# Kernel optimization log

Hardware: AMD Instinct MI355X
Metric: run time of the kernel (lower is better)

Reference implementation:

```python
import jax, jax.numpy as jnp
import numpy as np

NUM_GRAPHS = 100  # batch of graphs for pooling (dgl.max_nodes / WeightAndSum)


def _glorot(k, shape):
    lim = np.sqrt(6.0 / (shape[0] + shape[1])).astype(np.float32)
    return jax.random.uniform(k, shape, jnp.float32, -lim, lim)


def setup_inputs() -> dict:
    key = jax.random.key(0)
    ks = jax.random.split(key, 10)
    N, E, D, H = 100000, 1600000, 128, 128
    node_feats = jax.random.normal(ks[0], (N, D), dtype=jnp.float32)
    src = jax.random.randint(ks[1], (E,), 0, N, dtype=jnp.int32)
    dst = jax.random.randint(ks[2], (E,), 0, N, dtype=jnp.int32)
    graph_ids = jnp.sort(jax.random.randint(ks[3], (N,), 0, NUM_GRAPHS, dtype=jnp.int32))
    W1 = _glorot(ks[4], (D, H)); b1 = jnp.zeros((H,), jnp.float32)
    W2 = _glorot(ks[5], (H, H)); b2 = jnp.zeros((H,), jnp.float32)
    W3 = _glorot(ks[6], (H, H)); b3 = jnp.zeros((H,), jnp.float32)
    W_pool = _glorot(ks[7], (H, 1)); b_pool = jnp.zeros((1,), jnp.float32)
    return {"node_feats": node_feats, "src": src, "dst": dst, "graph_ids": graph_ids,
            "W1": W1, "b1": b1, "W2": W2, "b2": b2, "W3": W3, "b3": b3,
            "W_pool": W_pool, "b_pool": b_pool}


def _gcn_layer(h, W, b, src, dst, norm_src, norm_dst, N):
    # DGL GraphConv, norm='both': D_dst^{-1/2} (A^T (D_src^{-1/2} X W)) + b
    h = (h * norm_src[:, None]) @ W                      # [N, H]
    agg = jax.ops.segment_sum(h[src], dst, num_segments=N)  # gather + scatter-add
    return agg * norm_dst[:, None] + b


def reference(node_feats, src, dst, graph_ids, W1, b1, W2, b2, W3, b3, W_pool, b_pool):
    N = node_feats.shape[0]
    # dgl.add_self_loop (allow_zero_in_degree=False)
    loops = jnp.arange(N, dtype=src.dtype)
    src_sl = jnp.concatenate([src, loops])
    dst_sl = jnp.concatenate([dst, loops])
    ones = jnp.ones(src_sl.shape, jnp.float32)
    out_deg = jax.ops.segment_sum(ones, src_sl, num_segments=N)
    in_deg = jax.ops.segment_sum(ones, dst_sl, num_segments=N)
    norm_src = jax.lax.rsqrt(jnp.maximum(out_deg, 1.0))
    norm_dst = jax.lax.rsqrt(jnp.maximum(in_deg, 1.0))
    h = node_feats
    for W, b in ((W1, b1), (W2, b2), (W3, b3)):
        h = jax.nn.relu(_gcn_layer(h, W, b, src_sl, dst_sl, norm_src, norm_dst, N))
    # pooling_func: WeightAndSum (sigmoid-gated weighted sum per graph) + max_nodes
    w = jax.nn.sigmoid(h @ W_pool + b_pool)              # [N, 1]
    g_sum = jax.ops.segment_sum(h * w, graph_ids, num_segments=NUM_GRAPHS)
    g_max = jax.ops.segment_max(h, graph_ids, num_segments=NUM_GRAPHS)
    return jnp.concatenate([g_sum, g_max], axis=1)       # [G, 2H]
```

## Files before the change

kernel.cpp:

```cpp
#include <hip/hip_runtime.h>
#include <hip/hip_bf16.h>

#define DIM 128
#define CAP 64

typedef __attribute__((ext_vector_type(8))) short bf16x8;
typedef __attribute__((ext_vector_type(4))) float f32x4;
union U16 { uint4 u; bf16x8 b; };

__device__ __forceinline__ unsigned short f2bf(float f) {
    unsigned u = __float_as_uint(f);
    unsigned r = (u + 0x7fffu + ((u >> 16) & 1u)) >> 16;
    return (unsigned short)r;
}
__device__ __forceinline__ unsigned pack2bf(float a, float b) {
    return (unsigned)f2bf(a) | ((unsigned)f2bf(b) << 16);
}
__device__ __forceinline__ float2 unpack2bf(unsigned v) {
    float2 r;
    r.x = __uint_as_float(v << 16);
    r.y = __uint_as_float(v & 0xffff0000u);
    return r;
}
__device__ __forceinline__ void accum8s(float* acc, uint4 v, float s) {
    float2 f0 = unpack2bf(v.x), f1 = unpack2bf(v.y);
    float2 f2 = unpack2bf(v.z), f3 = unpack2bf(v.w);
    acc[0] += s * f0.x; acc[1] += s * f0.y; acc[2] += s * f1.x; acc[3] += s * f1.y;
    acc[4] += s * f2.x; acc[5] += s * f2.y; acc[6] += s * f3.x; acc[7] += s * f3.y;
}

__global__ __launch_bounds__(256) void k_build_gemm(const int* __restrict__ src,
                                                    const int* __restrict__ dst,
                                                    int* __restrict__ in_cnt,
                                                    int* __restrict__ out_cnt,
                                                    int* __restrict__ csr_pad, int E,
                                                    const float* __restrict__ x,
                                                    const float* __restrict__ W,
                                                    unsigned* __restrict__ xwb, int N,
                                                    int buildGrid, int mmGrid) {
    if (blockIdx.x & 1) {
        int bid = blockIdx.x >> 1;
        if (bid >= buildGrid) return;
        int e0 = (bid * 256 + threadIdx.x) * 4;
        int s[4], d[4], pos[4];
#pragma unroll
        for (int i = 0; i < 4; i++) {
            int e = e0 + i;
            if (e < E) { s[i] = src[e]; d[i] = dst[e]; }
        }
#pragma unroll
        for (int i = 0; i < 4; i++) {
            if (e0 + i < E) atomicAdd(&out_cnt[s[i]], 1);
        }
#pragma unroll
        for (int i = 0; i < 4; i++) {
            if (e0 + i < E) pos[i] = atomicAdd(&in_cnt[d[i]], 1);
        }
#pragma unroll
        for (int i = 0; i < 4; i++) {
            if (e0 + i < E && pos[i] < CAP) csr_pad[d[i] * CAP + pos[i]] = s[i];
        }
        return;
    }
    int bid = blockIdx.x >> 1;
    if (bid >= mmGrid) return;
    __shared__ float sW[32][128];
    __shared__ float sX[32][64];
    int t = threadIdx.x;
    int ty = t >> 4;
    int tx = t & 15;
    int nodeBase = bid * 64;

    float acc[4][8];
#pragma unroll
    for (int m = 0; m < 4; m++)
#pragma unroll
        for (int j = 0; j < 8; j++) acc[m][j] = 0.f;

    int ln = t & 63;
    int kb = (t >> 6) * 8;
    int nd = nodeBase + ln;

#pragma unroll 1
    for (int kc = 0; kc < DIM; kc += 32) {
#pragma unroll
        for (int i = 0; i < 4; i++) {
            int v = t + i * 256;
            int kk = v >> 5;
            int cc = (v & 31) * 4;
            *(float4*)&sW[kk][cc] = *(const float4*)&W[(kc + kk) * DIM + cc];
        }
        float4 a0, a1;
        if (nd < N) {
            a0 = *(const float4*)&x[nd * DIM + kc + kb];
            a1 = *(const float4*)&x[nd * DIM + kc + kb + 4];
        } else {
            a0 = make_float4(0, 0, 0, 0);
            a1 = make_float4(0, 0, 0, 0);
        }
        sX[kb + 0][ln] = a0.x;
        sX[kb + 1][ln] = a0.y;
        sX[kb + 2][ln] = a0.z;
        sX[kb + 3][ln] = a0.w;
        sX[kb + 4][ln] = a1.x;
        sX[kb + 5][ln] = a1.y;
        sX[kb + 6][ln] = a1.z;
        sX[kb + 7][ln] = a1.w;
        __syncthreads();

#pragma unroll
        for (int k = 0; k < 32; k++) {
            float4 xv = *(float4*)&sX[k][ty * 4];
            float4 wa = *(float4*)&sW[k][tx * 4];
            float4 wb = *(float4*)&sW[k][tx * 4 + 64];
            float xm[4] = {xv.x, xv.y, xv.z, xv.w};
#pragma unroll
            for (int m = 0; m < 4; m++) {
                acc[m][0] += xm[m] * wa.x;
                acc[m][1] += xm[m] * wa.y;
                acc[m][2] += xm[m] * wa.z;
                acc[m][3] += xm[m] * wa.w;
                acc[m][4] += xm[m] * wb.x;
                acc[m][5] += xm[m] * wb.y;
                acc[m][6] += xm[m] * wb.z;
                acc[m][7] += xm[m] * wb.w;
            }
        }
        __syncthreads();
    }

#pragma unroll
    for (int m = 0; m < 4; m++) {
        int n2 = nodeBase + ty * 4 + m;
        if (n2 < N) {
            uint2 q0, q1;
            q0.x = pack2bf(acc[m][0], acc[m][1]);
            q0.y = pack2bf(acc[m][2], acc[m][3]);
            q1.x = pack2bf(acc[m][4], acc[m][5]);
            q1.y = pack2bf(acc[m][6], acc[m][7]);
            *(uint2*)&xwb[n2 * 64 + tx * 2] = q0;
            *(uint2*)&xwb[n2 * 64 + 32 + tx * 2] = q1;
        }
    }
}

__global__ __launch_bounds__(256) void k_xw_mfma(const unsigned* __restrict__ hb,
                                                 const int* __restrict__ out_cnt,
                                                 const float* __restrict__ W,
                                                 unsigned* __restrict__ xwb, int N) {
    __shared__ unsigned wT[128 * 68];
    int t = threadIdx.x;
    {
        int n = t >> 1;
        int kp0 = (t & 1) * 32;
#pragma unroll
        for (int i = 0; i < 32; i++) {
            int kp = kp0 + i;
            wT[n * 68 + kp] = pack2bf(W[(2 * kp) * DIM + n], W[(2 * kp + 1) * DIM + n]);
        }
    }
    __syncthreads();
    int wave = t >> 6, lane = t & 63;
    int quad = lane >> 4, c = lane & 15;
    int m = blockIdx.x * 64 + wave * 16 + c;
    bool mv = m < N;
    f32x4 acc[8];
#pragma unroll
    for (int i = 0; i < 8; i++) acc[i] = (f32x4){0.f, 0.f, 0.f, 0.f};

#pragma unroll
    for (int ks = 0; ks < 4; ks++) {
        U16 av;
        if (mv) av.u = *(const uint4*)&hb[m * 64 + ks * 16 + quad * 4];
        else av.u = make_uint4(0, 0, 0, 0);
#pragma unroll
        for (int cb = 0; cb < 8; cb++) {
            U16 bv;
            bv.u = *(const uint4*)&wT[(cb * 16 + c) * 68 + ks * 16 + quad * 4];
            acc[cb] = __builtin_amdgcn_mfma_f32_16x16x32_bf16(av.b, bv.b, acc[cb], 0, 0, 0);
        }
    }
    int rowBase = blockIdx.x * 64 + wave * 16 + quad * 4;
#pragma unroll
    for (int r = 0; r < 4; r++) {
        int rowN = rowBase + r;
        float nrm = (rowN < N) ? rsqrtf((float)(out_cnt[rowN] + 1)) : 0.f;
#pragma unroll
        for (int cb = 0; cb < 8; cb++) {
            float v = acc[cb][r] * nrm;
            float vn = __shfl_xor(v, 1, 64);
            if (((c & 1) == 0) && rowN < N)
                xwb[rowN * 64 + cb * 8 + (c >> 1)] = pack2bf(v, vn);
        }
    }
}

template <bool GATED, bool SRCSCALE>
__device__ __forceinline__ void agg_body(const uint4* __restrict__ xwb4,
                                         const int* __restrict__ in_cnt,
                                         const int* __restrict__ out_cnt,
                                         const int* __restrict__ csr_pad,
                                         const float* __restrict__ bias,
                                         uint4* __restrict__ hb4,
                                         const float* __restrict__ Wp,
                                         const float* __restrict__ bp,
                                         float* __restrict__ wg, int N) {
    int gid = blockIdx.x * blockDim.x + threadIdx.x;
    int n = gid >> 6;
    int lane = gid & 63;
    if (n >= N) return;
    int quad = lane >> 4;
    int c = lane & 15;

    float acc[8];
#pragma unroll
    for (int i = 0; i < 8; i++) acc[i] = 0.f;

    if (quad == 0) {
        float sn = SRCSCALE ? rsqrtf((float)(out_cnt[n] + 1)) : 1.f;
        accum8s(acc, xwb4[n * 16 + c], sn);
    }
    int deg_true = in_cnt[n];
    int deg = deg_true > CAP ? CAP : deg_true;
    const int* row = &csr_pad[n * CAP];
    int p = 0;
    for (; p + 16 <= deg; p += 16) {
        int s0 = row[p + quad];
        int s1 = row[p + 4 + quad];
        int s2 = row[p + 8 + quad];
        int s3 = row[p + 12 + quad];
        uint4 v0 = xwb4[s0 * 16 + c];
        uint4 v1 = xwb4[s1 * 16 + c];
        uint4 v2 = xwb4[s2 * 16 + c];
        uint4 v3 = xwb4[s3 * 16 + c];
        float n0 = 1.f, n1 = 1.f, n2 = 1.f, n3 = 1.f;
        if (SRCSCALE) {
            int c0 = out_cnt[s0], c1 = out_cnt[s1], c2 = out_cnt[s2], c3 = out_cnt[s3];
            n0 = rsqrtf((float)(c0 + 1));
            n1 = rsqrtf((float)(c1 + 1));
            n2 = rsqrtf((float)(c2 + 1));
            n3 = rsqrtf((float)(c3 + 1));
        }
        accum8s(acc, v0, n0);
        accum8s(acc, v1, n1);
        accum8s(acc, v2, n2);
        accum8s(acc, v3, n3);
    }
    for (; p + 8 <= deg; p += 8) {
        int s0 = row[p + quad];
        int s1 = row[p + 4 + quad];
        uint4 v0 = xwb4[s0 * 16 + c];
        uint4 v1 = xwb4[s1 * 16 + c];
        float n0 = 1.f, n1 = 1.f;
        if (SRCSCALE) {
            int c0 = out_cnt[s0], c1 = out_cnt[s1];
            n0 = rsqrtf((float)(c0 + 1));
            n1 = rsqrtf((float)(c1 + 1));
        }
        accum8s(acc, v0, n0);
        accum8s(acc, v1, n1);
    }
    for (; p < deg; p += 4) {
        int pe = p + quad;
        int s = row[pe < deg ? pe : p];
        uint4 v = xwb4[s * 16 + c];
        float ns = SRCSCALE ? rsqrtf((float)(out_cnt[s] + 1)) : 1.f;
        if (pe < deg) accum8s(acc, v, ns);
    }
#pragma unroll
    for (int i = 0; i < 8; i++) {
        acc[i] += __shfl_xor(acc[i], 16, 64);
        acc[i] += __shfl_xor(acc[i], 32, 64);
    }
    float ndv = rsqrtf((float)(deg_true + 1));
    float4 b0 = ((const float4*)bias)[2 * c];
    float4 b1 = ((const float4*)bias)[2 * c + 1];
    float o[8];
    o[0] = fmaxf(acc[0] * ndv + b0.x, 0.f);
    o[1] = fmaxf(acc[1] * ndv + b0.y, 0.f);
    o[2] = fmaxf(acc[2] * ndv + b0.z, 0.f);
    o[3] = fmaxf(acc[3] * ndv + b0.w, 0.f);
    o[4] = fmaxf(acc[4] * ndv + b1.x, 0.f);
    o[5] = fmaxf(acc[5] * ndv + b1.y, 0.f);
    o[6] = fmaxf(acc[6] * ndv + b1.z, 0.f);
    o[7] = fmaxf(acc[7] * ndv + b1.w, 0.f);
    if (quad == 0) {
        uint4 w;
        w.x = pack2bf(o[0], o[1]);
        w.y = pack2bf(o[2], o[3]);
        w.z = pack2bf(o[4], o[5]);
        w.w = pack2bf(o[6], o[7]);
        hb4[n * 16 + c] = w;
    }
    if (GATED) {
        float s = 0.f;
        if (quad == 0) {
            float4 w0 = ((const float4*)Wp)[2 * c];
            float4 w1 = ((const float4*)Wp)[2 * c + 1];
            s = o[0] * w0.x + o[1] * w0.y + o[2] * w0.z + o[3] * w0.w +
                o[4] * w1.x + o[5] * w1.y + o[6] * w1.z + o[7] * w1.w;
        }
        s += __shfl_xor(s, 1, 64);
        s += __shfl_xor(s, 2, 64);
        s += __shfl_xor(s, 4, 64);
        s += __shfl_xor(s, 8, 64);
        if (lane == 0) wg[n] = 1.f / (1.f + expf(-(s + bp[0])));
    }
}

__global__ __launch_bounds__(256) void k_agg1(const uint4* __restrict__ xwb4,
                                              const int* __restrict__ in_cnt,
                                              const int* __restrict__ out_cnt,
                                              const int* __restrict__ csr_pad,
                                              const float* __restrict__ bias,
                                              uint4* __restrict__ hb4, int N) {
    agg_body<false, true>(xwb4, in_cnt, out_cnt, csr_pad, bias, hb4, nullptr, nullptr,
                          nullptr, N);
}

__global__ __launch_bounds__(256) void k_agg(const uint4* __restrict__ xwb4,
                                             const int* __restrict__ in_cnt,
                                             const int* __restrict__ csr_pad,
                                             const float* __restrict__ bias,
                                             uint4* __restrict__ hb4, int N) {
    agg_body<false, false>(xwb4, in_cnt, nullptr, csr_pad, bias, hb4, nullptr, nullptr,
                           nullptr, N);
}

__global__ __launch_bounds__(256) void k_agg_gate(const uint4* __restrict__ xwb4,
                                                  const int* __restrict__ in_cnt,
                                                  const int* __restrict__ csr_pad,
                                                  const float* __restrict__ bias,
                                                  uint4* __restrict__ hb4,
                                                  const float* __restrict__ Wp,
                                                  const float* __restrict__ bp,
                                                  float* __restrict__ wg, int N) {
    agg_body<true, false>(xwb4, in_cnt, nullptr, csr_pad, bias, hb4, Wp, bp, wg, N);
}

__device__ __forceinline__ int lower_bound(const int* a, int n, int key) {
    int lo = 0, hi = n;
    while (lo < hi) {
        int m = (lo + hi) >> 1;
        if (a[m] < key) lo = m + 1;
        else hi = m;
    }
    return lo;
}

__global__ __launch_bounds__(64) void k_pool(const unsigned* __restrict__ hb,
                                             const float* __restrict__ wg,
                                             const int* __restrict__ gids,
                                             float* __restrict__ out, int N) {
    int g = blockIdx.x >> 4;
    int part = blockIdx.x & 15;
    int t = threadIdx.x;
    int start = lower_bound(gids, N, g);
    int end = lower_bound(gids, N, g + 1);
    float2 sum = {0.f, 0.f}, mx = {0.f, 0.f};
    for (int n = start + part; n < end; n += 16) {
        float w = wg[n];
        float2 v = unpack2bf(hb[n * 64 + t]);
        sum.x += v.x * w;
        sum.y += v.y * w;
        mx.x = fmaxf(mx.x, v.x);
        mx.y = fmaxf(mx.y, v.y);
    }
    atomicAdd(&out[g * 256 + 2 * t], sum.x);
    atomicAdd(&out[g * 256 + 2 * t + 1], sum.y);
    atomicMax((int*)&out[g * 256 + 128 + 2 * t], __float_as_int(mx.x));
    atomicMax((int*)&out[g * 256 + 128 + 2 * t + 1], __float_as_int(mx.y));
}

extern "C" void kernel_launch(void* const* d_in, const int* in_sizes, int n_in,
                              void* d_out, int out_size, void* d_ws, size_t ws_size,
                              hipStream_t stream) {
    const float* node_feats = (const float*)d_in[0];
    const int* src = (const int*)d_in[1];
    const int* dst = (const int*)d_in[2];
    const int* gids = (const int*)d_in[3];
    const float* W1 = (const float*)d_in[4];
    const float* b1 = (const float*)d_in[5];
    const float* W2 = (const float*)d_in[6];
    const float* b2 = (const float*)d_in[7];
    const float* W3 = (const float*)d_in[8];
    const float* b3 = (const float*)d_in[9];
    const float* Wp = (const float*)d_in[10];
    const float* bp = (const float*)d_in[11];
    float* out = (float*)d_out;

    const int N = in_sizes[3];
    const int E = in_sizes[1];
    const int G = out_size / 256;

    char* ws = (char*)d_ws;
    size_t o = 0;
    int* in_cnt = (int*)(ws + o);        o += (size_t)N * 4;
    int* out_cnt = (int*)(ws + o);       o += (size_t)N * 4;
    size_t zero_bytes = o;
    float* wg = (float*)(ws + o);        o += (size_t)N * 4;
    o = (o + 15) & ~15ull;
    int* csr_pad = (int*)(ws + o);       o += (size_t)N * CAP * 4;
    unsigned* xwb = (unsigned*)(ws + o); o += (size_t)N * 64 * 4;
    unsigned* hb = (unsigned*)(ws + o);  o += (size_t)N * 64 * 4;
    (void)ws_size;

    (void)hipMemsetAsync(d_ws, 0, zero_bytes, stream);
    (void)hipMemsetAsync(d_out, 0, (size_t)out_size * 4, stream);

    int buildGrid = ((E + 3) / 4 + 255) / 256;
    int mmGrid = (N + 63) / 64;
    int aggGrid = ((N * 64) + 255) / 256;
    int fusedGrid = 2 * (buildGrid > mmGrid ? buildGrid : mmGrid);

    k_build_gemm<<<fusedGrid, 256, 0, stream>>>(src, dst, in_cnt, out_cnt, csr_pad, E,
                                                node_feats, W1, xwb, N, buildGrid, mmGrid);

    k_agg1<<<aggGrid, 256, 0, stream>>>((const uint4*)xwb, in_cnt, out_cnt, csr_pad, b1,
                                        (uint4*)hb, N);
    k_xw_mfma<<<mmGrid, 256, 0, stream>>>(hb, out_cnt, W2, xwb, N);
    k_agg<<<aggGrid, 256, 0, stream>>>((const uint4*)xwb, in_cnt, csr_pad, b2,
                                       (uint4*)hb, N);
    k_xw_mfma<<<mmGrid, 256, 0, stream>>>(hb, out_cnt, W3, xwb, N);
    k_agg_gate<<<aggGrid, 256, 0, stream>>>((const uint4*)xwb, in_cnt, csr_pad, b3,
                                            (uint4*)hb, Wp, bp, wg, N);

    k_pool<<<G * 16, 64, 0, stream>>>(hb, wg, gids, out, N);
}
```

Measured before the change: 508.9 us.

## Fuse aggregation and GEMM for layers 2-3 using aggregate-then-transform order

For layers 2 and 3 the order becomes aggregate-first then multiply: each block gathers neighbour rows of the previous bf16 activations (scaled by the source norm), stages 64 aggregated rows in shared memory, then runs the MFMA GEMM with W and applies dst norm, bias, ReLU and optional gating in the epilogue. This removes the separate xw kernels and one full N x 128 intermediate write and read per layer. In exchange each block handles 64 nodes with 4 waves looping serially, so there is less parallelism for the latency-bound gather. The per-edge out_cnt loads and rsqrt now also appear in layers 2 and 3. The aggregated sums are also rounded to bf16 before the GEMM.

```diff
diff --git a/kernel.cpp b/kernel.cpp
--- a/kernel.cpp
+++ b/kernel.cpp
@@ -144,67 +144,12 @@
     }
 }
 
-__global__ __launch_bounds__(256) void k_xw_mfma(const unsigned* __restrict__ hb,
-                                                 const int* __restrict__ out_cnt,
-                                                 const float* __restrict__ W,
-                                                 unsigned* __restrict__ xwb, int N) {
-    __shared__ unsigned wT[128 * 68];
-    int t = threadIdx.x;
-    {
-        int n = t >> 1;
-        int kp0 = (t & 1) * 32;
-#pragma unroll
-        for (int i = 0; i < 32; i++) {
-            int kp = kp0 + i;
-            wT[n * 68 + kp] = pack2bf(W[(2 * kp) * DIM + n], W[(2 * kp + 1) * DIM + n]);
-        }
-    }
-    __syncthreads();
-    int wave = t >> 6, lane = t & 63;
-    int quad = lane >> 4, c = lane & 15;
-    int m = blockIdx.x * 64 + wave * 16 + c;
-    bool mv = m < N;
-    f32x4 acc[8];
-#pragma unroll
-    for (int i = 0; i < 8; i++) acc[i] = (f32x4){0.f, 0.f, 0.f, 0.f};
-
-#pragma unroll
-    for (int ks = 0; ks < 4; ks++) {
-        U16 av;
-        if (mv) av.u = *(const uint4*)&hb[m * 64 + ks * 16 + quad * 4];
-        else av.u = make_uint4(0, 0, 0, 0);
-#pragma unroll
-        for (int cb = 0; cb < 8; cb++) {
-            U16 bv;
-            bv.u = *(const uint4*)&wT[(cb * 16 + c) * 68 + ks * 16 + quad * 4];
-            acc[cb] = __builtin_amdgcn_mfma_f32_16x16x32_bf16(av.b, bv.b, acc[cb], 0, 0, 0);
-        }
-    }
-    int rowBase = blockIdx.x * 64 + wave * 16 + quad * 4;
-#pragma unroll
-    for (int r = 0; r < 4; r++) {
-        int rowN = rowBase + r;
-        float nrm = (rowN < N) ? rsqrtf((float)(out_cnt[rowN] + 1)) : 0.f;
-#pragma unroll
-        for (int cb = 0; cb < 8; cb++) {
-            float v = acc[cb][r] * nrm;
-            float vn = __shfl_xor(v, 1, 64);
-            if (((c & 1) == 0) && rowN < N)
-                xwb[rowN * 64 + cb * 8 + (c >> 1)] = pack2bf(v, vn);
-        }
-    }
-}
-
-template <bool GATED, bool SRCSCALE>
-__device__ __forceinline__ void agg_body(const uint4* __restrict__ xwb4,
-                                         const int* __restrict__ in_cnt,
-                                         const int* __restrict__ out_cnt,
-                                         const int* __restrict__ csr_pad,
-                                         const float* __restrict__ bias,
-                                         uint4* __restrict__ hb4,
-                                         const float* __restrict__ Wp,
-                                         const float* __restrict__ bp,
-                                         float* __restrict__ wg, int N) {
+__global__ __launch_bounds__(256) void k_agg1(const uint4* __restrict__ xwb4,
+                                              const int* __restrict__ in_cnt,
+                                              const int* __restrict__ out_cnt,
+                                              const int* __restrict__ csr_pad,
+                                              const float* __restrict__ bias,
+                                              uint4* __restrict__ hb4, int N) {
     int gid = blockIdx.x * blockDim.x + threadIdx.x;
     int n = gid >> 6;
     int lane = gid & 63;
@@ -217,7 +162,7 @@
     for (int i = 0; i < 8; i++) acc[i] = 0.f;
 
     if (quad == 0) {
-        float sn = SRCSCALE ? rsqrtf((float)(out_cnt[n] + 1)) : 1.f;
+        float sn = rsqrtf((float)(out_cnt[n] + 1));
         accum8s(acc, xwb4[n * 16 + c], sn);
     }
     int deg_true = in_cnt[n];
@@ -233,14 +178,10 @@
         uint4 v1 = xwb4[s1 * 16 + c];
         uint4 v2 = xwb4[s2 * 16 + c];
         uint4 v3 = xwb4[s3 * 16 + c];
-        float n0 = 1.f, n1 = 1.f, n2 = 1.f, n3 = 1.f;
-        if (SRCSCALE) {
-            int c0 = out_cnt[s0], c1 = out_cnt[s1], c2 = out_cnt[s2], c3 = out_cnt[s3];
-            n0 = rsqrtf((float)(c0 + 1));
-            n1 = rsqrtf((float)(c1 + 1));
-            n2 = rsqrtf((float)(c2 + 1));
-            n3 = rsqrtf((float)(c3 + 1));
-        }
+        float n0 = rsqrtf((float)(out_cnt[s0] + 1));
+        float n1 = rsqrtf((float)(out_cnt[s1] + 1));
+        float n2 = rsqrtf((float)(out_cnt[s2] + 1));
+        float n3 = rsqrtf((float)(out_cnt[s3] + 1));
         accum8s(acc, v0, n0);
         accum8s(acc, v1, n1);
         accum8s(acc, v2, n2);
@@ -251,12 +192,8 @@
         int s1 = row[p + 4 + quad];
         uint4 v0 = xwb4[s0 * 16 + c];
         uint4 v1 = xwb4[s1 * 16 + c];
-        float n0 = 1.f, n1 = 1.f;
-        if (SRCSCALE) {
-            int c0 = out_cnt[s0], c1 = out_cnt[s1];
-            n0 = rsqrtf((float)(c0 + 1));
-            n1 = rsqrtf((float)(c1 + 1));
-        }
+        float n0 = rsqrtf((float)(out_cnt[s0] + 1));
+        float n1 = rsqrtf((float)(out_cnt[s1] + 1));
         accum8s(acc, v0, n0);
         accum8s(acc, v1, n1);
     }
@@ -264,7 +201,7 @@
         int pe = p + quad;
         int s = row[pe < deg ? pe : p];
         uint4 v = xwb4[s * 16 + c];
-        float ns = SRCSCALE ? rsqrtf((float)(out_cnt[s] + 1)) : 1.f;
+        float ns = rsqrtf((float)(out_cnt[s] + 1));
         if (pe < deg) accum8s(acc, v, ns);
     }
 #pragma unroll
@@ -273,69 +210,159 @@
         acc[i] += __shfl_xor(acc[i], 32, 64);
     }
     float ndv = rsqrtf((float)(deg_true + 1));
-    float4 b0 = ((const float4*)bias)[2 * c];
-    float4 b1 = ((const float4*)bias)[2 * c + 1];
-    float o[8];
-    o[0] = fmaxf(acc[0] * ndv + b0.x, 0.f);
-    o[1] = fmaxf(acc[1] * ndv + b0.y, 0.f);
-    o[2] = fmaxf(acc[2] * ndv + b0.z, 0.f);
-    o[3] = fmaxf(acc[3] * ndv + b0.w, 0.f);
-    o[4] = fmaxf(acc[4] * ndv + b1.x, 0.f);
-    o[5] = fmaxf(acc[5] * ndv + b1.y, 0.f);
-    o[6] = fmaxf(acc[6] * ndv + b1.z, 0.f);
-    o[7] = fmaxf(acc[7] * ndv + b1.w, 0.f);
     if (quad == 0) {
+        float4 b0 = ((const float4*)bias)[2 * c];
+        float4 b1 = ((const float4*)bias)[2 * c + 1];
         uint4 w;
-        w.x = pack2bf(o[0], o[1]);
-        w.y = pack2bf(o[2], o[3]);
-        w.z = pack2bf(o[4], o[5]);
-        w.w = pack2bf(o[6], o[7]);
+        w.x = pack2bf(fmaxf(acc[0] * ndv + b0.x, 0.f), fmaxf(acc[1] * ndv + b0.y, 0.f));
+        w.y = pack2bf(fmaxf(acc[2] * ndv + b0.z, 0.f), fmaxf(acc[3] * ndv + b0.w, 0.f));
+        w.z = pack2bf(fmaxf(acc[4] * ndv + b1.x, 0.f), fmaxf(acc[5] * ndv + b1.y, 0.f));
+        w.w = pack2bf(fmaxf(acc[6] * ndv + b1.z, 0.f), fmaxf(acc[7] * ndv + b1.w, 0.f));
         hb4[n * 16 + c] = w;
     }
-    if (GATED) {
-        float s = 0.f;
+}
+
+template <bool GATED>
+__global__ __launch_bounds__(256) void k_fused(const unsigned* __restrict__ hin,
+                                               const int* __restrict__ in_cnt,
+                                               const int* __restrict__ out_cnt,
+                                               const int* __restrict__ csr_pad,
+                                               const float* __restrict__ W,
+                                               const float* __restrict__ bias,
+                                               unsigned* __restrict__ hout,
+                                               const float* __restrict__ Wp,
+                                               const float* __restrict__ bp,
+                                               float* __restrict__ wg, int N) {
+    __shared__ unsigned wT[128 * 68];
+    __shared__ unsigned rows[64 * 68];
+    int t = threadIdx.x;
+    {
+        int n = t >> 1;
+        int kp0 = (t & 1) * 32;
+#pragma unroll
+        for (int i = 0; i < 32; i++) {
+            int kp = kp0 + i;
+            wT[n * 68 + kp] = pack2bf(W[(2 * kp) * DIM + n], W[(2 * kp + 1) * DIM + n]);
+        }
+    }
+    int wave = t >> 6, lane = t & 63;
+    int quad = lane >> 4, c = lane & 15;
+    const uint4* h4 = (const uint4*)hin;
+
+#pragma unroll 1
+    for (int j = 0; j < 16; j++) {
+        int nl = wave + 4 * j;
+        int n = blockIdx.x * 64 + nl;
+        float acc[8];
+#pragma unroll
+        for (int i = 0; i < 8; i++) acc[i] = 0.f;
+        if (n < N) {
+            if (quad == 0) {
+                float sn = rsqrtf((float)(out_cnt[n] + 1));
+                accum8s(acc, h4[n * 16 + c], sn);
+            }
+            int deg = in_cnt[n];
+            if (deg > CAP) deg = CAP;
+            const int* row = &csr_pad[n * CAP];
+            int p = 0;
+            for (; p + 16 <= deg; p += 16) {
+                int s0 = row[p + quad];
+                int s1 = row[p + 4 + quad];
+                int s2 = row[p + 8 + quad];
+                int s3 = row[p + 12 + quad];
+                uint4 v0 = h4[s0 * 16 + c];
+                uint4 v1 = h4[s1 * 16 + c];
+                uint4 v2 = h4[s2 * 16 + c];
+                uint4 v3 = h4[s3 * 16 + c];
+                float n0 = rsqrtf((float)(out_cnt[s0] + 1));
+                float n1 = rsqrtf((float)(out_cnt[s1] + 1));
+                float n2 = rsqrtf((float)(out_cnt[s2] + 1));
+                float n3 = rsqrtf((float)(out_cnt[s3] + 1));
+                accum8s(acc, v0, n0);
+                accum8s(acc, v1, n1);
+                accum8s(acc, v2, n2);
+                accum8s(acc, v3, n3);
+            }
+            for (; p + 8 <= deg; p += 8) {
+                int s0 = row[p + quad];
+                int s1 = row[p + 4 + quad];
+                uint4 v0 = h4[s0 * 16 + c];
+                uint4 v1 = h4[s1 * 16 + c];
+                float n0 = rsqrtf((float)(out_cnt[s0] + 1));
+                float n1 = rsqrtf((float)(out_cnt[s1] + 1));
+                accum8s(acc, v0, n0);
+                accum8s(acc, v1, n1);
+            }
+            for (; p < deg; p += 4) {
+                int pe = p + quad;
+                int s = row[pe < deg ? pe : p];
+                uint4 v = h4[s * 16 + c];
+                float ns = rsqrtf((float)(out_cnt[s] + 1));
+                if (pe < deg) accum8s(acc, v, ns);
+            }
+        }
+#pragma unroll
+        for (int i = 0; i < 8; i++) {
+            acc[i] += __shfl_xor(acc[i], 16, 64);
+            acc[i] += __shfl_xor(acc[i], 32, 64);
+        }
         if (quad == 0) {
-            float4 w0 = ((const float4*)Wp)[2 * c];
-            float4 w1 = ((const float4*)Wp)[2 * c + 1];
-            s = o[0] * w0.x + o[1] * w0.y + o[2] * w0.z + o[3] * w0.w +
-                o[4] * w1.x + o[5] * w1.y + o[6] * w1.z + o[7] * w1.w;
-        }
-        s += __shfl_xor(s, 1, 64);
-        s += __shfl_xor(s, 2, 64);
-        s += __shfl_xor(s, 4, 64);
-        s += __shfl_xor(s, 8, 64);
-        if (lane == 0) wg[n] = 1.f / (1.f + expf(-(s + bp[0])));
-    }
-}
-
-__global__ __launch_bounds__(256) void k_agg1(const uint4* __restrict__ xwb4,
-                                              const int* __restrict__ in_cnt,
-                                              const int* __restrict__ out_cnt,
-                                              const int* __restrict__ csr_pad,
-                                              const float* __restrict__ bias,
-                                              uint4* __restrict__ hb4, int N) {
-    agg_body<false, true>(xwb4, in_cnt, out_cnt, csr_pad, bias, hb4, nullptr, nullptr,
-                          nullptr, N);
-}
-
-__global__ __launch_bounds__(256) void k_agg(const uint4* __restrict__ xwb4,
-                                             const int* __restrict__ in_cnt,
-                                             const int* __restrict__ csr_pad,
-                                             const float* __restrict__ bias,
-                                             uint4* __restrict__ hb4, int N) {
-    agg_body<false, false>(xwb4, in_cnt, nullptr, csr_pad, bias, hb4, nullptr, nullptr,
-                           nullptr, N);
-}
-
-__global__ __launch_bounds__(256) void k_agg_gate(const uint4* __restrict__ xwb4,
-                                                  const int* __restrict__ in_cnt,
-                                                  const int* __restrict__ csr_pad,
-                                                  const float* __restrict__ bias,
-                                                  uint4* __restrict__ hb4,
-                                                  const float* __restrict__ Wp,
-                                                  const float* __restrict__ bp,
-                                                  float* __restrict__ wg, int N) {
-    agg_body<true, false>(xwb4, in_cnt, nullptr, csr_pad, bias, hb4, Wp, bp, wg, N);
+            uint4 w;
+            w.x = pack2bf(acc[0], acc[1]);
+            w.y = pack2bf(acc[2], acc[3]);
+            w.z = pack2bf(acc[4], acc[5]);
+            w.w = pack2bf(acc[6], acc[7]);
+            *(uint4*)&rows[nl * 68 + c * 4] = w;
+        }
+    }
+    __syncthreads();
+
+    f32x4 acc[8];
+#pragma unroll
+    for (int i = 0; i < 8; i++) acc[i] = (f32x4){0.f, 0.f, 0.f, 0.f};
+#pragma unroll
+    for (int ks = 0; ks < 4; ks++) {
+        U16 av;
+        av.u = *(const uint4*)&rows[(wave * 16 + c) * 68 + ks * 16 + quad * 4];
+#pragma unroll
+        for (int cb = 0; cb < 8; cb++) {
+            U16 bv;
+            bv.u = *(const uint4*)&wT[(cb * 16 + c) * 68 + ks * 16 + quad * 4];
+            acc[cb] = __builtin_amdgcn_mfma_f32_16x16x32_bf16(av.b, bv.b, acc[cb], 0, 0, 0);
+        }
+    }
+    float bcol[8], wpcol[8];
+#pragma unroll
+    for (int cb = 0; cb < 8; cb++) {
+        bcol[cb] = bias[cb * 16 + c];
+        if (GATED) wpcol[cb] = Wp[cb * 16 + c];
+    }
+    int rowBase = blockIdx.x * 64 + wave * 16 + quad * 4;
+#pragma unroll
+    for (int r = 0; r < 4; r++) {
+        int rowN = rowBase + r;
+        bool valid = rowN < N;
+        float ndv = valid ? rsqrtf((float)(in_cnt[rowN] + 1)) : 0.f;
+        float o[8];
+#pragma unroll
+        for (int cb = 0; cb < 8; cb++) o[cb] = fmaxf(acc[cb][r] * ndv + bcol[cb], 0.f);
+#pragma unroll
+        for (int cb = 0; cb < 8; cb++) {
+            float vn = __shfl_xor(o[cb], 1, 64);
+            if (((c & 1) == 0) && valid)
+                hout[rowN * 64 + cb * 8 + (c >> 1)] = pack2bf(o[cb], vn);
+        }
+        if (GATED) {
+            float s = 0.f;
+#pragma unroll
+            for (int cb = 0; cb < 8; cb++) s += o[cb] * wpcol[cb];
+            s += __shfl_xor(s, 1, 64);
+            s += __shfl_xor(s, 2, 64);
+            s += __shfl_xor(s, 4, 64);
+            s += __shfl_xor(s, 8, 64);
+            if (c == 0 && valid) wg[rowN] = 1.f / (1.f + expf(-(s + bp[0])));
+        }
+    }
 }
 
 __device__ __forceinline__ int lower_bound(const int* a, int n, int key) {
@@ -401,8 +428,8 @@
     float* wg = (float*)(ws + o);        o += (size_t)N * 4;
     o = (o + 15) & ~15ull;
     int* csr_pad = (int*)(ws + o);       o += (size_t)N * CAP * 4;
-    unsigned* xwb = (unsigned*)(ws + o); o += (size_t)N * 64 * 4;
-    unsigned* hb = (unsigned*)(ws + o);  o += (size_t)N * 64 * 4;
+    unsigned* bufA = (unsigned*)(ws + o); o += (size_t)N * 64 * 4;
+    unsigned* bufB = (unsigned*)(ws + o); o += (size_t)N * 64 * 4;
     (void)ws_size;
 
     (void)hipMemsetAsync(d_ws, 0, zero_bytes, stream);
@@ -414,16 +441,12 @@
     int fusedGrid = 2 * (buildGrid > mmGrid ? buildGrid : mmGrid);
 
     k_build_gemm<<<fusedGrid, 256, 0, stream>>>(src, dst, in_cnt, out_cnt, csr_pad, E,
-                                                node_feats, W1, xwb, N, buildGrid, mmGrid);
-
-    k_agg1<<<aggGrid, 256, 0, stream>>>((const uint4*)xwb, in_cnt, out_cnt, csr_pad, b1,
-                                        (uint4*)hb, N);
-    k_xw_mfma<<<mmGrid, 256, 0, stream>>>(hb, out_cnt, W2, xwb, N);
-    k_agg<<<aggGrid, 256, 0, stream>>>((const uint4*)xwb, in_cnt, csr_pad, b2,
-                                       (uint4*)hb, N);
-    k_xw_mfma<<<mmGrid, 256, 0, stream>>>(hb, out_cnt, W3, xwb, N);
-    k_agg_gate<<<aggGrid, 256, 0, stream>>>((const uint4*)xwb, in_cnt, csr_pad, b3,
-                                            (uint4*)hb, Wp, bp, wg, N);
-
-    k_pool<<<G * 16, 64, 0, stream>>>(hb, wg, gids, out, N);
-}
+                                                node_feats, W1, bufA, N, buildGrid, mmGrid);
+    k_agg1<<<aggGrid, 256, 0, stream>>>((const uint4*)bufA, in_cnt, out_cnt, csr_pad, b1,
+                                        (uint4*)bufB, N);
+    k_fused<false><<<mmGrid, 256, 0, stream>>>(bufB, in_cnt, out_cnt, csr_pad, W2, b2,
+                                               bufA, nullptr, nullptr, nullptr, N);
+    k_fused<true><<<mmGrid, 256, 0, stream>>>(bufA, in_cnt, out_cnt, csr_pad, W3, b3,
+                                              bufB, Wp, bp, wg, N);
+    k_pool<<<G * 16, 64, 0, stream>>>(bufB, wg, gids, out, N);
+}
```

Measured after the change: 634.6 us. +24.7%, slower.
